# Performance work log

Measured on AMD Instinct MI355X. Metric: run time of the kernel, lower is better.

The kernel has to match this reference:

```python
import jax, jax.numpy as jnp
import numpy as np

B, N, D, H = 512, 200, 128, 8
DH = D // H
CLIP = 10.0
NEG = -1e9


def setup_inputs():
    ks = jax.random.split(jax.random.key(0), 10)
    s = 1.0 / float(np.sqrt(D))
    f32 = jnp.float32
    return {
        "x": jax.random.normal(ks[0], (2, B, N, N), f32),
        "rf": jax.random.uniform(ks[1], (B, 2), f32),
        "node_embeddings": jax.random.normal(ks[2], (B, N, D), f32),
        "graph_embedding": jax.random.normal(ks[3], (B, D), f32),
        "Wk1_w": jax.random.normal(ks[4], (D, D), f32) * s,
        "Wk1_b": jnp.zeros((D,), f32),
        "Wv_w": jax.random.normal(ks[5], (D, D), f32) * s,
        "Wk2_w": jax.random.normal(ks[6], (D, D), f32) * s,
        "Wout_w": jax.random.normal(ks[7], (D, D), f32) * s,
        "Wq_w": jax.random.normal(ks[8], (D, D + 2), f32) * s,
        "init_node": jnp.zeros((D,), f32),
    }


def _forward(x, rf, node_embeddings, Wk1_w, Wk1_b, Wv_w, Wk2_w, Wout_w, Wq_w, init_node):
    # static projections (compute_static)
    K1 = node_embeddings @ Wk1_w.T + Wk1_b  # [B,N,D]
    V = node_embeddings @ Wv_w.T
    K2 = node_embeddings @ Wk2_w.T
    K1h = K1.reshape(B, N, H, DH).transpose(0, 2, 1, 3)  # [B,H,N,DH]
    Vh = V.reshape(B, N, H, DH).transpose(0, 2, 1, 3)
    barange = jnp.arange(B)
    narange = jnp.arange(N)

    def step(carry, _):
        mask, ctx, end = carry  # mask [B,N] bool, ctx [B,2+D], end [B] bool
        Q1 = ctx @ Wq_w.T  # [B,D]  (Wq_step)
        qh = Q1.reshape(B, H, DH)
        scores = jnp.einsum('bhd,bhnd->bhn', qh, K1h) / jnp.sqrt(jnp.float32(DH))
        scores = jnp.where(mask[:, None, :], NEG, scores)
        attn = jax.nn.softmax(scores, axis=-1)
        mha = jnp.einsum('bhn,bhnd->bhd', attn, Vh).reshape(B, D)
        Q2 = mha @ Wout_w.T  # [B,D]
        logits = CLIP * jnp.tanh(jnp.einsum('bd,bnd->bn', Q2, K2) / jnp.sqrt(jnp.float32(D)))
        logits = jnp.where(mask, NEG, logits)
        log_p = jax.nn.log_softmax(logits, axis=-1)  # [B,N]
        nxt = jnp.argmax(log_p, axis=-1)  # greedy decode (deterministic)
        nxt = jnp.where(end, nxt, 0)  # once node 0 chosen, stay at 0
        cur_emb = node_embeddings[barange, nxt]  # [B,D]
        end = end & (nxt != 0)
        mask = mask | (narange[None, :] == nxt[:, None])
        ctx = jnp.concatenate([rf, cur_emb], axis=1)
        return (mask, ctx, end), (log_p, nxt)

    ctx0 = jnp.concatenate([rf, jnp.broadcast_to(init_node, (B, D))], axis=1)
    carry0 = (jnp.zeros((B, N), bool), ctx0, jnp.ones((B,), bool))
    _, (log_ps, tours) = jax.lax.scan(step, carry0, None, length=N)
    log_ps = log_ps.transpose(1, 0, 2)  # [B,N,N]
    pi = tours.T  # [B,N]

    # get_cost
    index = jnp.argmax(pi == 0, axis=1)  # first occurrence of stop node 0
    steps_mask = narange[None, :] < index[:, None]
    cols = pi * steps_mask
    sol = jnp.zeros((B, N), jnp.float32).at[barange[:, None], cols].set(1.0)
    f1 = jnp.einsum('bn,bnm,bm->b', sol, x[0], sol)[:, None, None]  # [B,1,1]
    f2 = jnp.einsum('bn,bnm,bm->b', sol, x[1], sol)[:, None, None]
    cost = -(f1 * rf[0, 0] + f2 * rf[0, 1]).squeeze()  # [B]

    # log-likelihood of tour, weighted by solution membership
    chosen = jnp.take_along_axis(log_ps, pi[:, :, None], axis=2)[:, :, 0]  # [B,N]
    w = jnp.take_along_axis(sol, pi, axis=1)
    ll = jnp.sum(chosen * w, axis=1)  # [B]
    return cost, f1, f2, ll, pi


def reference(x, rf, node_embeddings, graph_embedding, Wk1_w, Wk1_b, Wv_w, Wk2_w, Wout_w, Wq_w, init_node):
    return _forward(x, rf, node_embeddings, Wk1_w, Wk1_b, Wv_w, Wk2_w, Wout_w, Wq_w, init_node)
```

## Files before the change

kernel.cpp:

```cpp
#include <hip/hip_runtime.h>
#include <math.h>

#define NEGV (-1e9f)

#define OUT_F   0l
#define M_F     52428800l
#define QR_F    (M_F + 65536l)
#define QI_F    (QR_F + 65536l)
#define SOL_F   (QI_F + 65536l)
#define WS_FLOATS (SOL_F + 102400l)

typedef float f32x4 __attribute__((ext_vector_type(4)));

#define DPPF(x, ctrl, oldv) __int_as_float(__builtin_amdgcn_update_dpp( \
      __float_as_int(oldv), __float_as_int(x), ctrl, 0xF, 0xF, false))

__device__ __forceinline__ float wave_max(float x) {
  x = fmaxf(x, DPPF(x, 0x111, -INFINITY));
  x = fmaxf(x, DPPF(x, 0x112, -INFINITY));
  x = fmaxf(x, DPPF(x, 0x114, -INFINITY));
  x = fmaxf(x, DPPF(x, 0x118, -INFINITY));
  x = fmaxf(x, DPPF(x, 0x142, -INFINITY));
  x = fmaxf(x, DPPF(x, 0x143, -INFINITY));
  return __int_as_float(__builtin_amdgcn_readlane(__float_as_int(x), 63));
}
__device__ __forceinline__ float wave_sum(float x) {
  x = x + DPPF(x, 0x111, 0.f);
  x = x + DPPF(x, 0x112, 0.f);
  x = x + DPPF(x, 0x114, 0.f);
  x = x + DPPF(x, 0x118, 0.f);
  x = x + DPPF(x, 0x142, 0.f);
  x = x + DPPF(x, 0x143, 0.f);
  return __int_as_float(__builtin_amdgcn_readlane(__float_as_int(x), 63));
}

__global__ __launch_bounds__(256)
void build_M(const float* __restrict__ Wk1, const float* __restrict__ Wv,
             const float* __restrict__ Wk2, const float* __restrict__ Wout,
             const float* __restrict__ Wq, float* __restrict__ Mbuf) {
  int g = blockIdx.x * 256 + threadIdx.x;
  int j = g >> 9, c = g & 511;
  float val;
  if (c < 128) {
    val = Wk1[c * 128 + j];
  } else if (c < 256) {
    val = Wv[(c - 128) * 128 + j];
  } else if (c < 384) {
    int d = c - 256;
    float s = 0.f;
    for (int e = 0; e < 128; ++e) s += Wk2[e * 128 + j] * Wout[e * 128 + d];
    val = s;
  } else {
    val = Wq[(c - 384) * 130 + 2 + j];
  }
  Mbuf[j * 512 + c] = val;
}

__global__ __launch_bounds__(256)
void build_Q(const float* __restrict__ rf, const float* __restrict__ Wq,
             const float* __restrict__ initn, float* __restrict__ QR,
             float* __restrict__ QI) {
  int g = blockIdx.x * 256 + threadIdx.x;
  int b = g >> 7, d = g & 127;
  float qr = Wq[d * 130 + 0] * rf[b * 2 + 0] + Wq[d * 130 + 1] * rf[b * 2 + 1];
  float qi = qr;
  for (int j = 0; j < 128; ++j) qi += Wq[d * 130 + 2 + j] * initn[j];
  QR[g] = qr;
  QI[g] = qi;
}

__global__ __launch_bounds__(256)
void gemm_static(const float* __restrict__ emb, const float* __restrict__ Mbuf,
                 const float* __restrict__ bk1, const float* __restrict__ QR,
                 float* __restrict__ OUT) {
  int bid = blockIdx.x;
  int lo = bid & 7, hi = bid >> 3;
  int rt = lo + 8 * (hi % 200);
  int ct = hi / 200;
  int r0 = rt * 64, c0 = ct * 64;
  int t = threadIdx.x, ty = t >> 4, tx = t & 15;
  int row0 = r0 + ty * 4;
  int col  = c0 + tx * 4;
  float acc[4][4] = {};
  const float* mp = Mbuf + col;
  for (int kb = 0; kb < 32; ++kb) {
    int k = kb * 4;
    float4 b0 = *(const float4*)(mp + (long)(k + 0) * 512);
    float4 b1 = *(const float4*)(mp + (long)(k + 1) * 512);
    float4 b2 = *(const float4*)(mp + (long)(k + 2) * 512);
    float4 b3 = *(const float4*)(mp + (long)(k + 3) * 512);
    float bm[4][4] = {{b0.x,b0.y,b0.z,b0.w},{b1.x,b1.y,b1.z,b1.w},
                      {b2.x,b2.y,b2.z,b2.w},{b3.x,b3.y,b3.z,b3.w}};
    #pragma unroll
    for (int rr = 0; rr < 4; ++rr) {
      float4 a4 = *(const float4*)(emb + (long)(row0 + rr) * 128 + k);
      float av[4] = {a4.x, a4.y, a4.z, a4.w};
      #pragma unroll
      for (int i = 0; i < 4; ++i)
        #pragma unroll
        for (int cc = 0; cc < 4; ++cc)
          acc[rr][cc] += av[i] * bm[i][cc];
    }
  }
  float badd[4] = {0.f, 0.f, 0.f, 0.f};
  if (c0 < 128) {
    #pragma unroll
    for (int cc = 0; cc < 4; ++cc) badd[cc] = bk1[col + cc];
  }
  #pragma unroll
  for (int rr = 0; rr < 4; ++rr) {
    int row = row0 + rr;
    float v[4];
    #pragma unroll
    for (int cc = 0; cc < 4; ++cc) v[cc] = acc[rr][cc] + badd[cc];
    if (col >= 384) {
      int bb = row / 200;
      #pragma unroll
      for (int cc = 0; cc < 4; ++cc) v[cc] += QR[bb * 128 + (col - 384) + cc];
    }
    float4 v4; v4.x = v[0]; v4.y = v[1]; v4.z = v[2]; v4.w = v[3];
    *(float4*)(OUT + (long)row * 512 + col) = v4;
  }
}

__global__ void init_ctr(int* __restrict__ c) { *c = 0; }

__global__ __attribute__((amdgpu_flat_work_group_size(512, 512), amdgpu_waves_per_eu(2, 2)))
void decode512(const float* __restrict__ OUT, const float* __restrict__ QI,
               int* __restrict__ ctr, float* __restrict__ sol,
               float* __restrict__ out) {
  __shared__ __align__(16) float qall[201 * 128];
  __shared__ float sc[1600];
  __shared__ __align__(16) float mhal[128];
  __shared__ float lg[200];
  __shared__ int bci, bsel;

  const int t = threadIdx.x;
  const int lane = t & 63, wave = t >> 6;
  const int o = t >> 2, r4 = t & 3;
  const int mn = t >> 1, half = t & 1;
  const int vst  = (r4 == 0) ? 0 : (r4 == 1 ? 48 : (r4 == 2 ? 100 : 152));
  const bool mid = (r4 == 1) || (r4 == 2);

  float kreg[64], ureg[64], vreg[52];

  for (;;) {
    if (t == 0) bsel = atomicAdd(ctr, 1);
    __syncthreads();
    const int b = bsel;
    if (b >= 512) break;
    const float* outb = OUT + (long)b * 200 * 512;

    for (int f = t; f < 25728; f += 512) {
      int row = f >> 7, d = f & 127;
      qall[f] = (row < 200) ? outb[row * 512 + 384 + d] : QI[b * 128 + d];
    }
    if (t < 400) {
      const float* kp = outb + mn * 512 + 64 * half;
      const float* up = outb + mn * 512 + 256 + 64 * half;
      #pragma unroll
      for (int c = 0; c < 16; ++c)
        *(f32x4*)&kreg[c * 4] = *(const f32x4*)(kp + c * 4);
      #pragma unroll
      for (int c = 0; c < 16; ++c)
        *(f32x4*)&ureg[c * 4] = *(const f32x4*)(up + c * 4);
    }
    {
      const float* vp = outb + 128 + o;
      #pragma unroll
      for (int i = 0; i < 48; ++i) vreg[i] = vp[(vst + i) * 512];
      vreg[48] = mid ? vp[(vst + 48) * 512] : 0.f;
      vreg[49] = mid ? vp[(vst + 49) * 512] : 0.f;
      vreg[50] = mid ? vp[(vst + 50) * 512] : 0.f;
      vreg[51] = mid ? vp[(vst + 51) * 512] : 0.f;
    }

    int cur = 200;
    bool cmb = false;
    bool live = true, picked0 = false;
    float llsum = 0.f, chose = 0.f;

    __syncthreads();

    for (int st = 0; st < 200; ++st) {
      if (t < 400) {
        const float* qb = qall + cur * 128 + 64 * half;
        #pragma unroll
        for (int hh = 0; hh < 4; ++hh) {
          float s = 0.f;
          #pragma unroll
          for (int c = 0; c < 4; ++c) {
            f32x4 q4 = *(const f32x4*)(qb + hh * 16 + c * 4);
            s += q4[0] * kreg[hh * 16 + c * 4 + 0];
            s += q4[1] * kreg[hh * 16 + c * 4 + 1];
            s += q4[2] * kreg[hh * 16 + c * 4 + 2];
            s += q4[3] * kreg[hh * 16 + c * 4 + 3];
          }
          sc[(4 * half + hh) * 200 + mn] = cmb ? NEGV : s * 0.25f;
        }
      }
      __syncthreads();

      {
        float sv[4];
        float mx = -INFINITY;
        #pragma unroll
        for (int k = 0; k < 4; ++k) {
          int n = lane + 64 * k;
          float s = (n < 200) ? sc[wave * 200 + n] : -INFINITY;
          sv[k] = s;
          mx = fmaxf(mx, s);
        }
        float vmax = wave_max(mx);
        float ls = 0.f;
        #pragma unroll
        for (int k = 0; k < 4; ++k) { sv[k] = expf(sv[k] - vmax); ls += sv[k]; }
        ls = wave_sum(ls);
        #pragma unroll
        for (int k = 0; k < 4; ++k) {
          int n = lane + 64 * k;
          if (n < 200) sc[wave * 200 + n] = sv[k] / ls;
        }
      }

      {
        const float* ap = sc + wave * 200 + vst;
        float ac[4] = {0.f, 0.f, 0.f, 0.f};
        #pragma unroll
        for (int c = 0; c < 12; ++c) {
          f32x4 av = *(const f32x4*)(ap + c * 4);
          float s = av[0] * vreg[c * 4 + 0];
          s += av[1] * vreg[c * 4 + 1];
          s += av[2] * vreg[c * 4 + 2];
          s += av[3] * vreg[c * 4 + 3];
          ac[c & 3] += s;
        }
        if (mid) {
          f32x4 av = *(const f32x4*)(ap + 48);
          float s = av[0] * vreg[48];
          s += av[1] * vreg[49]; s += av[2] * vreg[50]; s += av[3] * vreg[51];
          ac[0] += s;
        }
        float a = (ac[0] + ac[1]) + (ac[2] + ac[3]);
        a += DPPF(a, 0xB1, 0.f);
        a += DPPF(a, 0x4E, 0.f);
        if (r4 == 0) mhal[o] = a;
      }
      __syncthreads();

      if (t < 400) {
        float ac[4] = {0.f, 0.f, 0.f, 0.f};
        #pragma unroll
        for (int c = 0; c < 16; ++c) {
          f32x4 mh = *(const f32x4*)&mhal[64 * half + c * 4];
          float s = mh[0] * ureg[c * 4 + 0];
          s += mh[1] * ureg[c * 4 + 1];
          s += mh[2] * ureg[c * 4 + 2];
          s += mh[3] * ureg[c * 4 + 3];
          ac[c & 3] += s;
        }
        float a = (ac[0] + ac[1]) + (ac[2] + ac[3]);
        a += DPPF(a, 0xB1, 0.f);
        if (half == 0) {
          float l = 10.f * tanhf(a / 11.313708498984761f);
          lg[mn] = cmb ? NEGV : l;
        }
      }
      __syncthreads();

      if (wave == 7) {
        float lv[4];
        float mx = -INFINITY;
        #pragma unroll
        for (int k = 0; k < 4; ++k) {
          int n = lane + 64 * k;
          lv[k] = (n < 200) ? lg[n] : -INFINITY;
          mx = fmaxf(mx, lv[k]);
        }
        float vmax = wave_max(mx);
        int bidx = -1;
        #pragma unroll
        for (int k = 0; k < 4; ++k) {
          unsigned long long bm =
              __ballot((lane + 64 * k < 200) && (lv[k] == vmax));
          if (bidx < 0 && bm != 0ull) bidx = k * 64 + (int)__builtin_ctzll(bm);
        }
        int nxt = live ? bidx : 0;
        float e = 0.f;
        #pragma unroll
        for (int k = 0; k < 4; ++k) e += expf(lv[k] - vmax);
        float se_ = wave_sum(e);
        float lse = logf(se_);
        if (t == 448) {
          chose = live ? (-lse) : ((lv[0] - vmax) - lse);
          out[2048 + (long)b * 200 + st] = (float)nxt;
          bci = nxt;
        }
      }
      __syncthreads();

      int nxt = bci;
      if (!live) {
        if (t == 448) llsum += chose * (float)(200 - st);
        for (int s2 = st + 1 + t; s2 < 200; s2 += 512)
          out[2048 + (long)b * 200 + s2] = 0.f;
        break;
      }
      if (t == 448) llsum += chose;
      if (t < 400 && nxt == mn) cmb = true;
      cur = nxt;
      if (nxt == 0) { live = false; picked0 = true; }
    }

    if (t == 448) out[1536 + b] = picked0 ? llsum : 0.f;
    if (t < 400 && half == 0) {
      float s = (mn == 0) ? 1.f : ((picked0 && cmb) ? 1.f : 0.f);
      sol[(long)b * 200 + mn] = s;
    }
    __syncthreads();
  }
}

__global__ __attribute__((amdgpu_flat_work_group_size(1024, 1024)))
void decode(const float* __restrict__ OUT, const float* __restrict__ QI,
            int* __restrict__ ctr, float* __restrict__ sol,
            float* __restrict__ out) {
  __shared__ __align__(16) float k1r[25600];
  __shared__ __align__(16) float at[1600];
  __shared__ __align__(16) float mhal[128];
  __shared__ float lg[200];
  __shared__ __align__(16) float qv[128];
  __shared__ __align__(16) float ul[12800];
  __shared__ int   bci;
  __shared__ int   bsel;

  const int t = threadIdx.x;
  const int lane = t & 63, wave = t >> 6;
  const int o = t >> 3, q8 = t & 7;
  const int m4 = t >> 2, j4 = t & 3;
  const int stq = (q8 * 25) & ~3;
  const int cq  = ((((q8 + 1) * 25) & ~3) - stq) >> 2;

  for (;;) {
    if (t == 0) bsel = atomicAdd(ctr, 1);
    __syncthreads();
    const int b = bsel;
    if (b >= 512) break;
    const float* outb = OUT + (long)b * 200 * 512;

    for (int p = 0; p < 25; ++p) {
      int f = p * 1024 + t;
      int n = f >> 7, d = f & 127;
      k1r[n * 128 + ((d + 4 * n) & 127)] = outb[n * 512 + d];
    }
    for (int f = t; f < 12800; f += 1024) {
      int m = f >> 6, c = f & 63;
      ul[m * 64 + ((c + 4 * m) & 63)] =
          outb[m * 512 + 256 + (c >> 4) * 32 + 16 + (c & 15)];
    }
    f32x4 vA = {}, vB = {}, vC = {}, vD = {}, vE = {}, vF = {}, vG = {};
    {
      const float* vp = outb + 128 + o;
      #pragma unroll
      for (int e = 0; e < 4; ++e) vA[e] = vp[(stq + 0 + e) * 512];
      #pragma unroll
      for (int e = 0; e < 4; ++e) vB[e] = vp[(stq + 4 + e) * 512];
      #pragma unroll
      for (int e = 0; e < 4; ++e) vC[e] = vp[(stq + 8 + e) * 512];
      #pragma unroll
      for (int e = 0; e < 4; ++e) vD[e] = vp[(stq + 12 + e) * 512];
      #pragma unroll
      for (int e = 0; e < 4; ++e) vE[e] = vp[(stq + 16 + e) * 512];
      #pragma unroll
      for (int e = 0; e < 4; ++e) vF[e] = vp[(stq + 20 + e) * 512];
      if (cq == 7) {
        #pragma unroll
        for (int e = 0; e < 4; ++e) vG[e] = vp[(stq + 24 + e) * 512];
      }
    }
    f32x4 urR0 = {}, urR1 = {}, urR2 = {}, urR3 = {};
    if (t < 800) {
      const float* up = outb + m4 * 512 + 256 + j4 * 32;
      urR0 = *(const f32x4*)(up + 4 * ((0 + j4) & 3));
      urR1 = *(const f32x4*)(up + 4 * ((1 + j4) & 3));
      urR2 = *(const f32x4*)(up + 4 * ((2 + j4) & 3));
      urR3 = *(const f32x4*)(up + 4 * ((3 + j4) & 3));
    }
    if (t < 128) qv[t] = QI[b * 128 + t];

    int mk = 0;
    bool cm = false;
    bool live = true, picked0 = false;
    float llsum = 0.f, chose = 0.f;

    __syncthreads();

    for (int st = 0; st < 200; ++st) {
      if (wave < 8) {
        const int hb = wave * 16;
        float acc[4] = {};
        #pragma unroll
        for (int hf = 0; hf < 2; ++hf) {
          f32x4 qa = *(const f32x4*)&qv[hb + hf * 8];
          f32x4 qb2 = *(const f32x4*)&qv[hb + hf * 8 + 4];
          #pragma unroll
          for (int k = 0; k < 4; ++k) {
            int n = lane + 64 * k;
            if (n < 200) {
              const float* kb = k1r + n * 128;
              int off  = (hb + hf * 8 + 4 * n) & 127;
              int off2 = (hb + hf * 8 + 4 + 4 * n) & 127;
              f32x4 kA = *(const f32x4*)(kb + off);
              f32x4 kB = *(const f32x4*)(kb + off2);
              float ah = qa[0] * kA[0];
              ah += qa[1] * kA[1]; ah += qa[2] * kA[2]; ah += qa[3] * kA[3];
              ah += qb2[0] * kB[0]; ah += qb2[1] * kB[1];
              ah += qb2[2] * kB[2]; ah += qb2[3] * kB[3];
              acc[k] += ah;
            }
          }
        }
        float sv[4];
        float mx = -INFINITY;
        #pragma unroll
        for (int k = 0; k < 4; ++k) {
          int n = lane + 64 * k;
          float s = -INFINITY;
          if (n < 200) {
            s = acc[k] * 0.25f;
            if (mk & (1 << k)) s = NEGV;
          }
          sv[k] = s;
          mx = fmaxf(mx, s);
        }
        float vmax = wave_max(mx);
        float ls = 0.f;
        #pragma unroll
        for (int k = 0; k < 4; ++k) { sv[k] = expf(sv[k] - vmax); ls += sv[k]; }
        ls = wave_sum(ls);
        #pragma unroll
        for (int k = 0; k < 4; ++k) {
          int n = lane + 64 * k;
          if (n < 200) at[wave * 200 + n] = sv[k] / ls;
        }
      }
      __syncthreads();

      {
        const int h2 = t >> 7;
        const float* ap = at + h2 * 200 + stq;
        float a = 0.f;
        f32x4 av;
        av = *(const f32x4*)(ap + 0);
        a += av[0]*vA[0]; a += av[1]*vA[1]; a += av[2]*vA[2]; a += av[3]*vA[3];
        av = *(const f32x4*)(ap + 4);
        a += av[0]*vB[0]; a += av[1]*vB[1]; a += av[2]*vB[2]; a += av[3]*vB[3];
        av = *(const f32x4*)(ap + 8);
        a += av[0]*vC[0]; a += av[1]*vC[1]; a += av[2]*vC[2]; a += av[3]*vC[3];
        av = *(const f32x4*)(ap + 12);
        a += av[0]*vD[0]; a += av[1]*vD[1]; a += av[2]*vD[2]; a += av[3]*vD[3];
        av = *(const f32x4*)(ap + 16);
        a += av[0]*vE[0]; a += av[1]*vE[1]; a += av[2]*vE[2]; a += av[3]*vE[3];
        av = *(const f32x4*)(ap + 20);
        a += av[0]*vF[0]; a += av[1]*vF[1]; a += av[2]*vF[2]; a += av[3]*vF[3];
        if (cq == 7) {
          av = *(const f32x4*)(ap + 24);
          a += av[0]*vG[0]; a += av[1]*vG[1]; a += av[2]*vG[2]; a += av[3]*vG[3];
        }
        a += DPPF(a, 0xB1, 0.f);
        a += DPPF(a, 0x4E, 0.f);
        a += DPPF(a, 0x141, 0.f);
        if (q8 == 0) mhal[o] = a;
      }
      __syncthreads();

      if (t < 800) {
        float a = 0.f;
        {
          f32x4 ml;
          ml = *(const f32x4*)&mhal[j4 * 32 + ((0 + j4) & 3) * 4];
          a += ml[0]*urR0[0]; a += ml[1]*urR0[1]; a += ml[2]*urR0[2]; a += ml[3]*urR0[3];
          ml = *(const f32x4*)&mhal[j4 * 32 + ((1 + j4) & 3) * 4];
          a += ml[0]*urR1[0]; a += ml[1]*urR1[1]; a += ml[2]*urR1[2]; a += ml[3]*urR1[3];
          ml = *(const f32x4*)&mhal[j4 * 32 + ((2 + j4) & 3) * 4];
          a += ml[0]*urR2[0]; a += ml[1]*urR2[1]; a += ml[2]*urR2[2]; a += ml[3]*urR2[3];
          ml = *(const f32x4*)&mhal[j4 * 32 + ((3 + j4) & 3) * 4];
          a += ml[0]*urR3[0]; a += ml[1]*urR3[1]; a += ml[2]*urR3[2]; a += ml[3]*urR3[3];
        }
        const int ubase = m4 * 64;
        #pragma unroll
        for (int c = 0; c < 4; ++c) {
          int ci = (c + j4) & 3;
          f32x4 mh = *(const f32x4*)&mhal[j4 * 32 + 16 + ci * 4];
          f32x4 uu = *(const f32x4*)&ul[ubase + ((j4 * 16 + ci * 4 + 4 * m4) & 63)];
          a += mh[0]*uu[0]; a += mh[1]*uu[1]; a += mh[2]*uu[2]; a += mh[3]*uu[3];
        }
        a += DPPF(a, 0xB1, 0.f);
        a += DPPF(a, 0x4E, 0.f);
        if (j4 == 0) {
          float l = 10.f * tanhf(a / 11.313708498984761f);
          lg[m4] = cm ? NEGV : l;
        }
      }
      __syncthreads();

      if (wave < 8) {
        float lv[4];
        float mx = -INFINITY;
        #pragma unroll
        for (int k = 0; k < 4; ++k) {
          int n = lane + 64 * k;
          lv[k] = (n < 200) ? lg[n] : -INFINITY;
          mx = fmaxf(mx, lv[k]);
        }
        float vmax = wave_max(mx);
        int bidx = -1;
        #pragma unroll
        for (int k = 0; k < 4; ++k) {
          unsigned long long bm =
              __ballot((lane + 64 * k < 200) && (lv[k] == vmax));
          if (bidx < 0 && bm != 0ull) bidx = k * 64 + (int)__builtin_ctzll(bm);
        }
        int nxt = live ? bidx : 0;
        if (t < 128) qv[t] = outb[(long)nxt * 512 + 384 + t];
        float e = 0.f;
        #pragma unroll
        for (int k = 0; k < 4; ++k) e += expf(lv[k] - vmax);
        float se_ = wave_sum(e);
        float lse = logf(se_);
        if (t == 0) {
          chose = live ? (-lse) : ((lv[0] - vmax) - lse);
          out[2048 + (long)b * 200 + st] = (float)nxt;
          bci = nxt;
        }
      }
      __syncthreads();

      int nxt = bci;
      if (!live) {
        if (t == 0) llsum += chose * (float)(200 - st);
        for (int s2 = st + 1 + t; s2 < 200; s2 += 1024)
          out[2048 + (long)b * 200 + s2] = 0.f;
        break;
      }
      if (t == 0) llsum += chose;
      if (wave < 8 && (nxt & 63) == lane) mk |= 1 << (nxt >> 6);
      if (t < 800 && nxt == m4) cm = true;
      if (nxt == 0) { live = false; picked0 = true; }
    }

    if (t == 0) out[1536 + b] = picked0 ? llsum : 0.f;
    if (t < 800 && j4 == 0) {
      float s = (m4 == 0) ? 1.f : ((picked0 && cm) ? 1.f : 0.f);
      sol[(long)b * 200 + m4] = s;
    }
    __syncthreads();
  }
}

__global__ __launch_bounds__(256)
void cost_kernel(const float* __restrict__ x, const float* __restrict__ rf,
                 const float* __restrict__ sol, float* __restrict__ out) {
  __shared__ float solL[256];
  __shared__ float red[8];
  const int b = blockIdx.x, t = threadIdx.x;
  solL[t] = (t < 200) ? sol[b * 200 + t] : 0.f;
  __syncthreads();
  const float* x0 = x + (long)b * 40000;
  const float* x1 = x + 20480000l + (long)b * 40000;
  float a1 = 0.f, a2 = 0.f;
  if (t < 200) {
    #pragma unroll 4
    for (int i = 0; i < 200; ++i) {
      float w2 = solL[i];
      a1 += x0[i * 200 + t] * w2;
      a2 += x1[i * 200 + t] * w2;
    }
    float w = solL[t];
    a1 *= w; a2 *= w;
  }
  #pragma unroll
  for (int off = 32; off > 0; off >>= 1) {
    a1 += __shfl_xor(a1, off);
    a2 += __shfl_xor(a2, off);
  }
  if ((t & 63) == 0) { red[(t >> 6) * 2] = a1; red[(t >> 6) * 2 + 1] = a2; }
  __syncthreads();
  if (t == 0) {
    float f1 = red[0] + red[2] + red[4] + red[6];
    float f2 = red[1] + red[3] + red[5] + red[7];
    out[b]        = -(f1 * rf[0] + f2 * rf[1]);
    out[512 + b]  = f1;
    out[1024 + b] = f2;
  }
}

extern "C" void kernel_launch(void* const* d_in, const int* in_sizes, int n_in,
                              void* d_out, int out_size, void* d_ws, size_t ws_size,
                              hipStream_t stream) {
  const float* x     = (const float*)d_in[0];
  const float* rf    = (const float*)d_in[1];
  const float* emb   = (const float*)d_in[2];
  const float* Wk1   = (const float*)d_in[4];
  const float* bk1   = (const float*)d_in[5];
  const float* Wv    = (const float*)d_in[6];
  const float* Wk2   = (const float*)d_in[7];
  const float* Wout  = (const float*)d_in[8];
  const float* Wq    = (const float*)d_in[9];
  const float* initn = (const float*)d_in[10];
  float* out = (float*)d_out;
  float* ws  = (float*)d_ws;

  if (ws_size < (size_t)WS_FLOATS * 4) return;

  float* OUTb = ws + OUT_F;
  float* Mb   = ws + M_F;
  float* QRb  = ws + QR_F;
  float* QIb  = ws + QI_F;
  float* solb = ws + SOL_F;

  build_M<<<256, 256, 0, stream>>>(Wk1, Wv, Wk2, Wout, Wq, Mb);
  build_Q<<<256, 256, 0, stream>>>(rf, Wq, initn, QRb, QIb);
  gemm_static<<<12800, 256, 0, stream>>>(emb, Mb, bk1, QRb, OUTb);
  init_ctr<<<1, 1, 0, stream>>>((int*)QRb);

  hipFuncAttributes fa;
  bool big = false;
  if (hipFuncGetAttributes(&fa, (const void*)decode512) == hipSuccess)
    big = (fa.localSizeBytes <= 64);
  if (big)
    decode512<<<256, 512, 0, stream>>>(OUTb, QIb, (int*)QRb, solb, out);
  else
    decode<<<256, 1024, 0, stream>>>(OUTb, QIb, (int*)QRb, solb, out);

  cost_kernel<<<512, 256, 0, stream>>>(x, rf, solb, out);
}
```

Measured before the change: 1.270 ms.

## Compute attention scores per-wave in registers, removing LDS round trip and barrier

Each wave now owns one head and computes the q·K1 scores for its 200 nodes directly in registers, with K1 slices reloaded per lane and the mask kept as a per-lane bitmask. This removes the shared-memory score write, one __syncthreads per decode step, and the re-read before the softmax. In exchange, each lane holds 64 K1 values laid out by node rather than by head, and all 512 threads take part in the score computation.

```diff
diff --git a/kernel.cpp b/kernel.cpp
--- a/kernel.cpp
+++ b/kernel.cpp
@@ -155,12 +155,21 @@
       int row = f >> 7, d = f & 127;
       qall[f] = (row < 200) ? outb[row * 512 + 384 + d] : QI[b * 128 + d];
     }
+    #pragma unroll
+    for (int k = 0; k < 4; ++k) {
+      int n = lane + 64 * k;
+      if (n < 200) {
+        const float* kp = outb + n * 512 + wave * 16;
+        #pragma unroll
+        for (int c = 0; c < 4; ++c)
+          *(f32x4*)&kreg[k * 16 + c * 4] = *(const f32x4*)(kp + c * 4);
+      } else {
+        #pragma unroll
+        for (int c = 0; c < 16; ++c) kreg[k * 16 + c] = 0.f;
+      }
+    }
     if (t < 400) {
-      const float* kp = outb + mn * 512 + 64 * half;
       const float* up = outb + mn * 512 + 256 + 64 * half;
-      #pragma unroll
-      for (int c = 0; c < 16; ++c)
-        *(f32x4*)&kreg[c * 4] = *(const f32x4*)(kp + c * 4);
       #pragma unroll
       for (int c = 0; c < 16; ++c)
         *(f32x4*)&ureg[c * 4] = *(const f32x4*)(up + c * 4);
@@ -176,6 +185,7 @@
     }
 
     int cur = 200;
+    int mk = 0;
     bool cmb = false;
     bool live = true, picked0 = false;
     float llsum = 0.f, chose = 0.f;
@@ -183,31 +193,38 @@
     __syncthreads();
 
     for (int st = 0; st < 200; ++st) {
-      if (t < 400) {
-        const float* qb = qall + cur * 128 + 64 * half;
-        #pragma unroll
-        for (int hh = 0; hh < 4; ++hh) {
-          float s = 0.f;
-          #pragma unroll
-          for (int c = 0; c < 4; ++c) {
-            f32x4 q4 = *(const f32x4*)(qb + hh * 16 + c * 4);
-            s += q4[0] * kreg[hh * 16 + c * 4 + 0];
-            s += q4[1] * kreg[hh * 16 + c * 4 + 1];
-            s += q4[2] * kreg[hh * 16 + c * 4 + 2];
-            s += q4[3] * kreg[hh * 16 + c * 4 + 3];
-          }
-          sc[(4 * half + hh) * 200 + mn] = cmb ? NEGV : s * 0.25f;
-        }
-      }
-      __syncthreads();
-
       {
+        const float* qb = qall + cur * 128 + wave * 16;
+        f32x4 q0 = *(const f32x4*)(qb + 0);
+        f32x4 q1 = *(const f32x4*)(qb + 4);
+        f32x4 q2 = *(const f32x4*)(qb + 8);
+        f32x4 q3 = *(const f32x4*)(qb + 12);
         float sv[4];
         float mx = -INFINITY;
         #pragma unroll
         for (int k = 0; k < 4; ++k) {
           int n = lane + 64 * k;
-          float s = (n < 200) ? sc[wave * 200 + n] : -INFINITY;
+          float s = -INFINITY;
+          if (n < 200) {
+            float a = q0[0] * kreg[k * 16 + 0];
+            a += q0[1] * kreg[k * 16 + 1];
+            a += q0[2] * kreg[k * 16 + 2];
+            a += q0[3] * kreg[k * 16 + 3];
+            a += q1[0] * kreg[k * 16 + 4];
+            a += q1[1] * kreg[k * 16 + 5];
+            a += q1[2] * kreg[k * 16 + 6];
+            a += q1[3] * kreg[k * 16 + 7];
+            a += q2[0] * kreg[k * 16 + 8];
+            a += q2[1] * kreg[k * 16 + 9];
+            a += q2[2] * kreg[k * 16 + 10];
+            a += q2[3] * kreg[k * 16 + 11];
+            a += q3[0] * kreg[k * 16 + 12];
+            a += q3[1] * kreg[k * 16 + 13];
+            a += q3[2] * kreg[k * 16 + 14];
+            a += q3[3] * kreg[k * 16 + 15];
+            s = a * 0.25f;
+            if (mk & (1 << k)) s = NEGV;
+          }
           sv[k] = s;
           mx = fmaxf(mx, s);
         }
@@ -307,6 +324,7 @@
         break;
       }
       if (t == 448) llsum += chose;
+      if ((nxt & 63) == lane) mk |= 1 << (nxt >> 6);
       if (t < 400 && nxt == mn) cmb = true;
       cur = nxt;
       if (nxt == 0) { live = false; picked0 = true; }
```

Result: faster. 1.215 ms (-4.3%).
